# Optimization experiments

Measured on AMD Instinct MI355X. Metric: run time of the kernel, lower is better.

Reference implementation:

```python
import jax, jax.numpy as jnp
import numpy as np
from jax import lax

CHUNK = 64          # rows per chunk in the parabola pass (bounds peak memory)
INF = jnp.float32(1e12)  # 'no site in this column' sentinel for squared distance


def _edt_sq(mask):
    """Exact squared Euclidean distance transform of a 2D bool mask.

    Matches scipy.ndimage.distance_transform_edt(mask)**2: for pixels where
    mask is True (nonzero), squared distance to the nearest False (zero)
    pixel; 0 at False pixels. Separable: 1D along-column distance, then a
    brute-force lower-envelope (parabola) pass along rows, which is exact.
    """
    h, w = mask.shape
    sites = ~mask  # zero pixels = distance sources
    idx = jnp.arange(h, dtype=jnp.int32)[:, None]  # [H,1]
    # distance (in rows) to nearest site above / below in the same column
    up = idx - lax.cummax(jnp.where(sites, idx, -h), axis=0)
    down = lax.cummin(jnp.where(sites, idx, 2 * h), axis=0, reverse=True) - idx
    d = jnp.minimum(up, down)  # >= h means no site in this column
    g = jnp.where(d >= h, INF, d.astype(jnp.float32) ** 2)  # [H,W]

    # parabola pass along axis 1: out[r, j] = min_k g[r, k] + (j-k)^2
    j = jnp.arange(w, dtype=jnp.float32)
    dk2 = (j[:, None] - j[None, :]) ** 2  # [W_j, W_k]

    def row_chunk(gc):  # gc: [CHUNK, W]
        return jnp.min(gc[:, None, :] + dk2[None, :, :], axis=-1)

    gch = g.reshape(h // CHUNK, CHUNK, w)
    return lax.map(row_chunk, gch).reshape(h, w)


def _signed_distance(t):
    """t: bool foreground mask. Returns inside*(~t) - (outside-1)*t, where
    outside = EDT(t) (fg pixel -> nearest bg) and inside = EDT(~t)
    (bg pixel -> nearest fg), as in the original distance_metric."""
    outside = jnp.sqrt(_edt_sq(t))
    inside = jnp.sqrt(_edt_sq(~t))
    tf = t.astype(jnp.float32)
    return inside * (1.0 - tf) - (outside - 1.0) * tf


def setup_inputs() -> dict:
    key = jax.random.key(0)
    k1, k2 = jax.random.split(key)
    inp = jax.random.normal(k1, (1024, 1024), dtype=jnp.float32)
    target = jax.random.randint(k2, (1024, 1024), 0, 2, dtype=jnp.int32)
    return {"input": inp, "target": target}


def reference(input, target):
    sd = _signed_distance(target != 0)
    return jnp.mean(input * sd)
```

## Files before the change

### kernel.cpp

```cpp
#include <hip/hip_runtime.h>

#define H 1024
#define W 1024
#define NPIX (H * W)
#define WW 16
#define INF_F 1e12f
#define THREADS 256
#define BIG (1 << 29)

__device__ __noinline__ int vert_dist_full(const unsigned long long* __restrict__ pw,
                                           int r, int c, int pol) {
  int w = r >> 6, b = r & 63;
  unsigned long long v = pw[w * W + c];
  unsigned long long m_c = pol ? v : ~v;
  int dup = 1 << 30, ddn = 1 << 30;
  unsigned long long am = m_c & ((1ULL << b) - 1ULL);
  if (am) {
    dup = b - (63 - __builtin_clzll(am));
  } else {
    for (int ww = w - 1; ww >= 0; --ww) {
      unsigned long long mv = pw[ww * W + c];
      mv = pol ? mv : ~mv;
      if (mv) { dup = r - (ww * 64 + 63 - __builtin_clzll(mv)); break; }
    }
  }
  unsigned long long bm = m_c >> b;
  if (bm) {
    ddn = __builtin_ctzll(bm);
  } else {
    for (int ww = w + 1; ww < WW; ++ww) {
      unsigned long long mv = pw[ww * W + c];
      mv = pol ? mv : ~mv;
      if (mv) { ddn = (ww * 64 + __builtin_ctzll(mv)) - r; break; }
    }
  }
  return min(dup, ddn);
}

__device__ __noinline__ int horiz_exact(const unsigned long long* __restrict__ pw,
                                        int r, int c, int pol, int best, int dk0) {
  for (int dk = dk0; dk < W; ++dk) {
    int dk2 = dk * dk;
    if (dk2 >= best) break;
    if (c - dk >= 0) {
      int d = vert_dist_full(pw, r, c - dk, pol);
      if (d < H) best = min(best, d * d + dk2);
    }
    if (c + dk < W) {
      int d = vert_dist_full(pw, r, c + dk, pol);
      if (d < H) best = min(best, d * d + dk2);
    }
  }
  return best;
}

__global__ __launch_bounds__(THREADS) void pack_bits(
    const int* __restrict__ target, unsigned int* __restrict__ pw32) {
  int tg = blockIdx.x * THREADS + threadIdx.x;
  int w = tg >> 11;
  int half = (tg >> 10) & 1;
  int c = tg & (W - 1);
  int rbase = w * 64 + half * 32;
  unsigned int val = 0;
#pragma unroll
  for (int b = 0; b < 32; ++b) {
    if (target[(rbase + b) * W + c] != 0) val |= (1u << b);
  }
  pw32[((w * W + c) << 1) + half] = val;
}

__global__ __launch_bounds__(THREADS) void fused_edt_row(
    const unsigned long long* __restrict__ pw,
    const float* __restrict__ input,
    double* __restrict__ partials) {
  __shared__ unsigned char sd8[2][W + 64];
  const int tid = threadIdx.x;
  const int r = blockIdx.x;
  const int w = r >> 6, b = r & 63;
  const int c0 = tid << 2;

  if (tid < 32) {
    int p = tid >> 4, q = tid & 15;
    ((unsigned int*)sd8)[p * 272 + (q < 8 ? q : 256 + q)] = 0xFFFFFFFFu;
  }

  unsigned long long curv[4], prevv[4], nextv[4];
  *(ulonglong2*)&curv[0] = *(const ulonglong2*)(pw + w * W + c0);
  *(ulonglong2*)&curv[2] = *(const ulonglong2*)(pw + w * W + c0 + 2);
  const bool hp = (w > 0), hn = (w < WW - 1);
  if (hp) {
    *(ulonglong2*)&prevv[0] = *(const ulonglong2*)(pw + (w - 1) * W + c0);
    *(ulonglong2*)&prevv[2] = *(const ulonglong2*)(pw + (w - 1) * W + c0 + 2);
  } else prevv[0] = prevv[1] = prevv[2] = prevv[3] = 0ULL;
  if (hn) {
    *(ulonglong2*)&nextv[0] = *(const ulonglong2*)(pw + (w + 1) * W + c0);
    *(ulonglong2*)&nextv[2] = *(const ulonglong2*)(pw + (w + 1) * W + c0 + 2);
  } else nextv[0] = nextv[1] = nextv[2] = nextv[3] = 0ULL;

  unsigned char dloc[2][4];
#pragma unroll
  for (int pol = 0; pol < 2; ++pol) {
#pragma unroll
    for (int k = 0; k < 4; ++k) {
      unsigned long long m_c = pol ? curv[k] : ~curv[k];
      unsigned long long m_p = hp ? (pol ? prevv[k] : ~prevv[k]) : 0ULL;
      unsigned long long m_n = hn ? (pol ? nextv[k] : ~nextv[k]) : 0ULL;
      int d = 1 << 30;
      unsigned long long am = m_c & ((1ULL << b) - 1ULL);
      if (am) d = b - (63 - __builtin_clzll(am));
      else if (m_p) d = b + 1 + __builtin_clzll(m_p);
      unsigned long long bm = m_c >> b;
      int dd = 1 << 30;
      if (bm) dd = __builtin_ctzll(bm);
      else if (m_n) dd = (64 - b) + __builtin_ctzll(m_n);
      d = min(d, dd);
      if (d > 64) d = vert_dist_full(pw, r, c0 + k, pol);
      dloc[pol][k] = (unsigned char)min(d, 255);
    }
  }
#pragma unroll
  for (int pol = 0; pol < 2; ++pol) {
    unsigned int u = (unsigned int)dloc[pol][0] |
                     ((unsigned int)dloc[pol][1] << 8) |
                     ((unsigned int)dloc[pol][2] << 16) |
                     ((unsigned int)dloc[pol][3] << 24);
    *(unsigned int*)&sd8[pol][32 + c0] = u;
  }
  __syncthreads();

  double val = 0.0;
  const float4 iv = *(const float4*)(input + r * W + c0);
  const float ivk[4] = {iv.x, iv.y, iv.z, iv.w};
#pragma unroll
  for (int k = 0; k < 4; ++k) {
    const bool t = (dloc[1][k] == 0);
    const int pol = t ? 0 : 1;
    const int own = dloc[pol][k];
    int best = (own == 255) ? BIG : own * own;
    const unsigned char* __restrict__ sg = &sd8[pol][32 + c0 + k];
#pragma unroll
    for (int dk = 1; dk <= 2; ++dk) {
      int dl = sg[-dk], dr = sg[dk];
      int gl = (dl == 255) ? BIG : dl * dl;
      int gr = (dr == 255) ? BIG : dr * dr;
      best = min(best, min(gl, gr) + dk * dk);
    }
    for (int dk = 3; dk <= 32; ++dk) {
      int dk2 = dk * dk;
      if (dk2 >= best) break;
      int dl = sg[-dk], dr = sg[dk];
      int gl = (dl == 255) ? BIG : dl * dl;
      int gr = (dr == 255) ? BIG : dr * dr;
      best = min(best, min(gl, gr) + dk2);
    }
    if (best > 1089) {
      int c = c0 + k;
      if (best > 65025) {
        int ov = vert_dist_full(pw, r, c, pol);
        best = (ov < H) ? ov * ov : (1 << 30);
        best = horiz_exact(pw, r, c, pol, best, 1);
      } else {
        best = horiz_exact(pw, r, c, pol, best, 33);
      }
    }
    float bestf = (best >= BIG) ? INF_F : (float)best;
    float dist = sqrtf(bestf);
    float sd = t ? (1.0f - dist) : dist;
    val += (double)(ivk[k] * sd);
  }

  for (int off = 32; off > 0; off >>= 1)
    val += __shfl_down(val, off, 64);
  __shared__ double smem[THREADS / 64];
  int lane = tid & 63, wid = tid >> 6;
  if (lane == 0) smem[wid] = val;
  __syncthreads();
  if (tid == 0)
    partials[blockIdx.x] = smem[0] + smem[1] + smem[2] + smem[3];
}

__global__ __launch_bounds__(THREADS) void reduce_partials(
    const double* __restrict__ partials, float* __restrict__ out) {
  double s = 0.0;
#pragma unroll
  for (int i = 0; i < 4; ++i) s += partials[threadIdx.x + i * THREADS];
  for (int off = 32; off > 0; off >>= 1)
    s += __shfl_down(s, off, 64);
  __shared__ double smem[THREADS / 64];
  int lane = threadIdx.x & 63, wid = threadIdx.x >> 6;
  if (lane == 0) smem[wid] = s;
  __syncthreads();
  if (threadIdx.x == 0)
    out[0] = (float)((smem[0] + smem[1] + smem[2] + smem[3]) / (double)NPIX);
}

extern "C" void kernel_launch(void* const* d_in, const int* in_sizes, int n_in,
                              void* d_out, int out_size, void* d_ws, size_t ws_size,
                              hipStream_t stream) {
  const float* input = (const float*)d_in[0];
  const int* target = (const int*)d_in[1];
  float* out = (float*)d_out;

  double* partials = (double*)d_ws;
  unsigned long long* pw = (unsigned long long*)((char*)d_ws + 8192);

  pack_bits<<<128, THREADS, 0, stream>>>(target, (unsigned int*)pw);
  fused_edt_row<<<H, THREADS, 0, stream>>>(pw, input, partials);
  reduce_partials<<<1, THREADS, 0, stream>>>(partials, out);
}
```

Before: 66.21 us.

## Fuse pack, EDT and reduction into one cooperative kernel with two rows per block

```diff
diff --git a/kernel.cpp b/kernel.cpp
--- a/kernel.cpp
+++ b/kernel.cpp
@@ -1,4 +1,7 @@
 #include <hip/hip_runtime.h>
+#include <hip/hip_cooperative_groups.h>
+
+namespace cg = cooperative_groups;
 
 #define H 1024
 #define W 1024
@@ -6,6 +9,7 @@
 #define WW 16
 #define INF_F 1e12f
 #define THREADS 256
+#define BLOCKS 512
 #define BIG (1 << 29)
 
 __device__ __noinline__ int vert_dist_full(const unsigned long long* __restrict__ pw,
@@ -54,32 +58,44 @@
   return best;
 }
 
-__global__ __launch_bounds__(THREADS) void pack_bits(
-    const int* __restrict__ target, unsigned int* __restrict__ pw32) {
-  int tg = blockIdx.x * THREADS + threadIdx.x;
-  int w = tg >> 11;
-  int half = (tg >> 10) & 1;
-  int c = tg & (W - 1);
-  int rbase = w * 64 + half * 32;
-  unsigned int val = 0;
-#pragma unroll
-  for (int b = 0; b < 32; ++b) {
-    if (target[(rbase + b) * W + c] != 0) val |= (1u << b);
-  }
-  pw32[((w * W + c) << 1) + half] = val;
-}
-
-__global__ __launch_bounds__(THREADS) void fused_edt_row(
-    const unsigned long long* __restrict__ pw,
+__global__ __launch_bounds__(THREADS, 2) void fused_all(
+    const int* __restrict__ target,
     const float* __restrict__ input,
-    double* __restrict__ partials) {
-  __shared__ unsigned char sd8[2][W + 64];
+    unsigned long long* __restrict__ pw,
+    double* __restrict__ partials,
+    unsigned int* __restrict__ count,
+    float* __restrict__ out) {
   const int tid = threadIdx.x;
-  const int r = blockIdx.x;
-  const int w = r >> 6, b = r & 63;
+  const int bid = blockIdx.x;
+
+  if (bid == 0 && tid == 0) *count = 0u;
+
+  if (tid < 64) {
+    int tg = (bid << 6) + tid;
+    int w = tg >> 11;
+    int half = (tg >> 10) & 1;
+    int c = tg & (W - 1);
+    int rbase = w * 64 + half * 32;
+    unsigned int val = 0;
+#pragma unroll
+    for (int b = 0; b < 32; ++b) {
+      if (target[(rbase + b) * W + c] != 0) val |= (1u << b);
+    }
+    ((unsigned int*)pw)[((w * W + c) << 1) + half] = val;
+  }
+
+  cg::this_grid().sync();
+
+  __shared__ unsigned char sd8[2][2][W + 64];
+  __shared__ double smem[THREADS / 64];
+  __shared__ int amLast;
+
+  const int r0 = bid << 1;
+  const int w = r0 >> 6;
+  const int b0 = r0 & 63;
   const int c0 = tid << 2;
 
-  if (tid < 32) {
+  if (tid < 64) {
     int p = tid >> 4, q = tid & 15;
     ((unsigned int*)sd8)[p * 272 + (q < 8 ? q : 256 + q)] = 0xFFFFFFFFu;
   }
@@ -97,7 +113,7 @@
     *(ulonglong2*)&nextv[2] = *(const ulonglong2*)(pw + (w + 1) * W + c0 + 2);
   } else nextv[0] = nextv[1] = nextv[2] = nextv[3] = 0ULL;
 
-  unsigned char dloc[2][4];
+  unsigned char dloc[2][2][4];
 #pragma unroll
   for (int pol = 0; pol < 2; ++pol) {
 #pragma unroll
@@ -105,93 +121,104 @@
       unsigned long long m_c = pol ? curv[k] : ~curv[k];
       unsigned long long m_p = hp ? (pol ? prevv[k] : ~prevv[k]) : 0ULL;
       unsigned long long m_n = hn ? (pol ? nextv[k] : ~nextv[k]) : 0ULL;
-      int d = 1 << 30;
-      unsigned long long am = m_c & ((1ULL << b) - 1ULL);
-      if (am) d = b - (63 - __builtin_clzll(am));
-      else if (m_p) d = b + 1 + __builtin_clzll(m_p);
-      unsigned long long bm = m_c >> b;
-      int dd = 1 << 30;
-      if (bm) dd = __builtin_ctzll(bm);
-      else if (m_n) dd = (64 - b) + __builtin_ctzll(m_n);
-      d = min(d, dd);
-      if (d > 64) d = vert_dist_full(pw, r, c0 + k, pol);
-      dloc[pol][k] = (unsigned char)min(d, 255);
-    }
-  }
-#pragma unroll
-  for (int pol = 0; pol < 2; ++pol) {
-    unsigned int u = (unsigned int)dloc[pol][0] |
-                     ((unsigned int)dloc[pol][1] << 8) |
-                     ((unsigned int)dloc[pol][2] << 16) |
-                     ((unsigned int)dloc[pol][3] << 24);
-    *(unsigned int*)&sd8[pol][32 + c0] = u;
+#pragma unroll
+      for (int rr = 0; rr < 2; ++rr) {
+        int b = b0 + rr;
+        int d = 1 << 30;
+        unsigned long long am = m_c & ((1ULL << b) - 1ULL);
+        if (am) d = b - (63 - __builtin_clzll(am));
+        else if (m_p) d = b + 1 + __builtin_clzll(m_p);
+        unsigned long long bm = m_c >> b;
+        int dd = 1 << 30;
+        if (bm) dd = __builtin_ctzll(bm);
+        else if (m_n) dd = (64 - b) + __builtin_ctzll(m_n);
+        d = min(d, dd);
+        if (d > 64) d = vert_dist_full(pw, r0 + rr, c0 + k, pol);
+        dloc[rr][pol][k] = (unsigned char)min(d, 255);
+      }
+    }
+  }
+#pragma unroll
+  for (int rr = 0; rr < 2; ++rr) {
+#pragma unroll
+    for (int pol = 0; pol < 2; ++pol) {
+      unsigned int u = (unsigned int)dloc[rr][pol][0] |
+                       ((unsigned int)dloc[rr][pol][1] << 8) |
+                       ((unsigned int)dloc[rr][pol][2] << 16) |
+                       ((unsigned int)dloc[rr][pol][3] << 24);
+      *(unsigned int*)&sd8[rr][pol][32 + c0] = u;
+    }
   }
   __syncthreads();
 
   double val = 0.0;
-  const float4 iv = *(const float4*)(input + r * W + c0);
-  const float ivk[4] = {iv.x, iv.y, iv.z, iv.w};
-#pragma unroll
-  for (int k = 0; k < 4; ++k) {
-    const bool t = (dloc[1][k] == 0);
-    const int pol = t ? 0 : 1;
-    const int own = dloc[pol][k];
-    int best = (own == 255) ? BIG : own * own;
-    const unsigned char* __restrict__ sg = &sd8[pol][32 + c0 + k];
-#pragma unroll
-    for (int dk = 1; dk <= 2; ++dk) {
-      int dl = sg[-dk], dr = sg[dk];
-      int gl = (dl == 255) ? BIG : dl * dl;
-      int gr = (dr == 255) ? BIG : dr * dr;
-      best = min(best, min(gl, gr) + dk * dk);
-    }
-    for (int dk = 3; dk <= 32; ++dk) {
-      int dk2 = dk * dk;
-      if (dk2 >= best) break;
-      int dl = sg[-dk], dr = sg[dk];
-      int gl = (dl == 255) ? BIG : dl * dl;
-      int gr = (dr == 255) ? BIG : dr * dr;
-      best = min(best, min(gl, gr) + dk2);
-    }
-    if (best > 1089) {
-      int c = c0 + k;
-      if (best > 65025) {
-        int ov = vert_dist_full(pw, r, c, pol);
-        best = (ov < H) ? ov * ov : (1 << 30);
-        best = horiz_exact(pw, r, c, pol, best, 1);
-      } else {
-        best = horiz_exact(pw, r, c, pol, best, 33);
-      }
-    }
-    float bestf = (best >= BIG) ? INF_F : (float)best;
-    float dist = sqrtf(bestf);
-    float sd = t ? (1.0f - dist) : dist;
-    val += (double)(ivk[k] * sd);
+#pragma unroll
+  for (int rr = 0; rr < 2; ++rr) {
+    const int r = r0 + rr;
+    const float4 iv = *(const float4*)(input + r * W + c0);
+    const float ivk[4] = {iv.x, iv.y, iv.z, iv.w};
+#pragma unroll
+    for (int k = 0; k < 4; ++k) {
+      const bool t = (dloc[rr][1][k] == 0);
+      const int pol = t ? 0 : 1;
+      const int own = dloc[rr][pol][k];
+      int best = (own == 255) ? BIG : own * own;
+      const unsigned char* __restrict__ sg = &sd8[rr][pol][32 + c0 + k];
+#pragma unroll
+      for (int dk = 1; dk <= 2; ++dk) {
+        int dl = sg[-dk], dr = sg[dk];
+        int gl = (dl == 255) ? BIG : dl * dl;
+        int gr = (dr == 255) ? BIG : dr * dr;
+        best = min(best, min(gl, gr) + dk * dk);
+      }
+      for (int dk = 3; dk <= 32; ++dk) {
+        int dk2 = dk * dk;
+        if (dk2 >= best) break;
+        int dl = sg[-dk], dr = sg[dk];
+        int gl = (dl == 255) ? BIG : dl * dl;
+        int gr = (dr == 255) ? BIG : dr * dr;
+        best = min(best, min(gl, gr) + dk2);
+      }
+      if (best > 1089) {
+        int c = c0 + k;
+        if (best > 65025) {
+          int ov = vert_dist_full(pw, r, c, pol);
+          best = (ov < H) ? ov * ov : (1 << 30);
+          best = horiz_exact(pw, r, c, pol, best, 1);
+        } else {
+          best = horiz_exact(pw, r, c, pol, best, 33);
+        }
+      }
+      float bestf = (best >= BIG) ? INF_F : (float)best;
+      float dist = sqrtf(bestf);
+      float sd = t ? (1.0f - dist) : dist;
+      val += (double)(ivk[k] * sd);
+    }
   }
 
   for (int off = 32; off > 0; off >>= 1)
     val += __shfl_down(val, off, 64);
-  __shared__ double smem[THREADS / 64];
   int lane = tid & 63, wid = tid >> 6;
   if (lane == 0) smem[wid] = val;
   __syncthreads();
-  if (tid == 0)
-    partials[blockIdx.x] = smem[0] + smem[1] + smem[2] + smem[3];
-}
-
-__global__ __launch_bounds__(THREADS) void reduce_partials(
-    const double* __restrict__ partials, float* __restrict__ out) {
-  double s = 0.0;
-#pragma unroll
-  for (int i = 0; i < 4; ++i) s += partials[threadIdx.x + i * THREADS];
-  for (int off = 32; off > 0; off >>= 1)
-    s += __shfl_down(s, off, 64);
-  __shared__ double smem[THREADS / 64];
-  int lane = threadIdx.x & 63, wid = threadIdx.x >> 6;
-  if (lane == 0) smem[wid] = s;
+  if (tid == 0) {
+    partials[bid] = smem[0] + smem[1] + smem[2] + smem[3];
+    __threadfence();
+    unsigned int old = atomicAdd(count, 1u);
+    amLast = (old == BLOCKS - 1);
+  }
   __syncthreads();
-  if (threadIdx.x == 0)
-    out[0] = (float)((smem[0] + smem[1] + smem[2] + smem[3]) / (double)NPIX);
+  if (amLast) {
+    __threadfence();
+    double s = partials[tid] + partials[tid + THREADS];
+    for (int off = 32; off > 0; off >>= 1)
+      s += __shfl_down(s, off, 64);
+    if (lane == 0) smem[wid] = s;
+    __syncthreads();
+    if (tid == 0)
+      out[0] = (float)((smem[0] + smem[1] + smem[2] + smem[3]) /
+                       (double)NPIX);
+  }
 }
 
 extern "C" void kernel_launch(void* const* d_in, const int* in_sizes, int n_in,
@@ -202,9 +229,11 @@
   float* out = (float*)d_out;
 
   double* partials = (double*)d_ws;
+  unsigned int* count = (unsigned int*)((char*)d_ws + 4096);
   unsigned long long* pw = (unsigned long long*)((char*)d_ws + 8192);
 
-  pack_bits<<<128, THREADS, 0, stream>>>(target, (unsigned int*)pw);
-  fused_edt_row<<<H, THREADS, 0, stream>>>(pw, input, partials);
-  reduce_partials<<<1, THREADS, 0, stream>>>(partials, out);
-}
+  void* args[] = {(void*)&target, (void*)&input, (void*)&pw,
+                  (void*)&partials, (void*)&count, (void*)&out};
+  hipLaunchCooperativeKernel((const void*)fused_all, dim3(BLOCKS), dim3(THREADS),
+                             args, 0, stream);
+}
```

After: 120.5 us. +82.0%, slower.

## Fuse final reduction via fixed-point atomics and widen bit-packing grid

Applied to the files above, without the earlier changes.

```diff
diff --git a/kernel.cpp b/kernel.cpp
--- a/kernel.cpp
+++ b/kernel.cpp
@@ -6,7 +6,9 @@
 #define WW 16
 #define INF_F 1e12f
 #define THREADS 256
+#define RBLOCKS H
 #define BIG (1 << 29)
+#define FXSCALE 1048576.0
 
 __device__ __noinline__ int vert_dist_full(const unsigned long long* __restrict__ pw,
                                            int r, int c, int pol) {
@@ -55,29 +57,37 @@
 }
 
 __global__ __launch_bounds__(THREADS) void pack_bits(
-    const int* __restrict__ target, unsigned int* __restrict__ pw32) {
+    const int* __restrict__ target, unsigned short* __restrict__ pw16,
+    unsigned int* __restrict__ count, unsigned long long* __restrict__ acc) {
+  if (blockIdx.x == 0 && threadIdx.x == 0) { *count = 0u; *acc = 0ULL; }
   int tg = blockIdx.x * THREADS + threadIdx.x;
-  int w = tg >> 11;
-  int half = (tg >> 10) & 1;
   int c = tg & (W - 1);
-  int rbase = w * 64 + half * 32;
+  int rest = tg >> 10;
+  int w = rest >> 2;
+  int quarter = rest & 3;
+  int rbase = w * 64 + quarter * 16;
   unsigned int val = 0;
 #pragma unroll
-  for (int b = 0; b < 32; ++b) {
+  for (int b = 0; b < 16; ++b) {
     if (target[(rbase + b) * W + c] != 0) val |= (1u << b);
   }
-  pw32[((w * W + c) << 1) + half] = val;
+  pw16[((w * W + c) << 2) + quarter] = (unsigned short)val;
 }
 
 __global__ __launch_bounds__(THREADS) void fused_edt_row(
     const unsigned long long* __restrict__ pw,
     const float* __restrict__ input,
-    double* __restrict__ partials) {
+    unsigned int* __restrict__ count,
+    unsigned long long* __restrict__ acc,
+    float* __restrict__ out) {
   __shared__ unsigned char sd8[2][W + 64];
+  __shared__ double smem[THREADS / 64];
   const int tid = threadIdx.x;
   const int r = blockIdx.x;
   const int w = r >> 6, b = r & 63;
   const int c0 = tid << 2;
+
+  const float4 iv = *(const float4*)(input + r * W + c0);
 
   if (tid < 32) {
     int p = tid >> 4, q = tid & 15;
@@ -129,7 +139,6 @@
   __syncthreads();
 
   double val = 0.0;
-  const float4 iv = *(const float4*)(input + r * W + c0);
   const float ivk[4] = {iv.x, iv.y, iv.z, iv.w};
 #pragma unroll
   for (int k = 0; k < 4; ++k) {
@@ -171,27 +180,21 @@
 
   for (int off = 32; off > 0; off >>= 1)
     val += __shfl_down(val, off, 64);
-  __shared__ double smem[THREADS / 64];
   int lane = tid & 63, wid = tid >> 6;
   if (lane == 0) smem[wid] = val;
   __syncthreads();
-  if (tid == 0)
-    partials[blockIdx.x] = smem[0] + smem[1] + smem[2] + smem[3];
-}
-
-__global__ __launch_bounds__(THREADS) void reduce_partials(
-    const double* __restrict__ partials, float* __restrict__ out) {
-  double s = 0.0;
-#pragma unroll
-  for (int i = 0; i < 4; ++i) s += partials[threadIdx.x + i * THREADS];
-  for (int off = 32; off > 0; off >>= 1)
-    s += __shfl_down(s, off, 64);
-  __shared__ double smem[THREADS / 64];
-  int lane = threadIdx.x & 63, wid = threadIdx.x >> 6;
-  if (lane == 0) smem[wid] = s;
-  __syncthreads();
-  if (threadIdx.x == 0)
-    out[0] = (float)((smem[0] + smem[1] + smem[2] + smem[3]) / (double)NPIX);
+  if (tid == 0) {
+    double bval = smem[0] + smem[1] + smem[2] + smem[3];
+    long long fx = llrint(bval * FXSCALE);
+    unsigned long long prev = atomicAdd(acc, (unsigned long long)fx);
+    asm volatile("" ::"v"(prev) : "memory");
+    unsigned int old = atomicAdd(count, 1u);
+    if (old == RBLOCKS - 1) {
+      unsigned long long tot = atomicAdd(acc, 0ULL);
+      double total = (double)(long long)tot * (1.0 / FXSCALE);
+      out[0] = (float)(total / (double)NPIX);
+    }
+  }
 }
 
 extern "C" void kernel_launch(void* const* d_in, const int* in_sizes, int n_in,
@@ -201,10 +204,10 @@
   const int* target = (const int*)d_in[1];
   float* out = (float*)d_out;
 
-  double* partials = (double*)d_ws;
+  unsigned int* count = (unsigned int*)d_ws;
+  unsigned long long* acc = (unsigned long long*)((char*)d_ws + 128);
   unsigned long long* pw = (unsigned long long*)((char*)d_ws + 8192);
 
-  pack_bits<<<128, THREADS, 0, stream>>>(target, (unsigned int*)pw);
-  fused_edt_row<<<H, THREADS, 0, stream>>>(pw, input, partials);
-  reduce_partials<<<1, THREADS, 0, stream>>>(partials, out);
-}
+  pack_bits<<<256, THREADS, 0, stream>>>(target, (unsigned short*)pw, count, acc);
+  fused_edt_row<<<RBLOCKS, THREADS, 0, stream>>>(pw, input, count, acc, out);
+}
```

New measurement: 83.44 us. +26.0%, slower.
